# Optimization experiments

Hardware: AMD Instinct MI355X
Metric: run time of the kernel (lower is better)

Reference implementation:

```python
import jax, jax.numpy as jnp
import numpy as np

N_NODES = 50000
N_EDGES = 1600000
IN_CH, HID_CH, OUT_CH = 256, 128, 64


def setup_inputs() -> dict:
    key = jax.random.key(0)
    k1, k2, k3, k4 = jax.random.split(key, 4)
    x = jax.random.normal(k1, (N_NODES, IN_CH), dtype=jnp.float32)
    edge_index = jax.random.randint(k2, (2, N_EDGES), 0, N_NODES, dtype=jnp.int64)
    # Glorot-style init for weights, zero bias (as PyG GCNConv)
    W1 = jax.random.normal(k3, (IN_CH, HID_CH), dtype=jnp.float32) * (1.0 / np.sqrt(IN_CH))
    b1 = jnp.zeros((HID_CH,), dtype=jnp.float32)
    W2 = jax.random.normal(k4, (HID_CH, OUT_CH), dtype=jnp.float32) * (1.0 / np.sqrt(HID_CH))
    b2 = jnp.zeros((OUT_CH,), dtype=jnp.float32)
    return {"x": x, "edge_index": edge_index, "W1": W1, "b1": b1, "W2": W2, "b2": b2}


def _gcn_norm(edge_index, num_nodes):
    # PyG GCNConv default: add self-loops, symmetric normalization deg^-1/2 A deg^-1/2
    loop = jnp.arange(num_nodes, dtype=edge_index.dtype)
    src = jnp.concatenate([edge_index[0], loop])
    dst = jnp.concatenate([edge_index[1], loop])
    deg = jax.ops.segment_sum(jnp.ones_like(dst, dtype=jnp.float32), dst, num_segments=num_nodes)
    dinv = jnp.where(deg > 0, jax.lax.rsqrt(jnp.maximum(deg, 1.0)), 0.0)
    norm = dinv[src] * dinv[dst]  # [E + N]
    return src, dst, norm


def _gcn_conv(x, src, dst, norm, W, b, num_nodes):
    h = x @ W                              # [N, C_out] dense GEMM first (PyG order)
    msg = h[src] * norm[:, None]           # gather + scale, [E+N, C_out]
    out = jax.ops.segment_sum(msg, dst, num_segments=num_nodes)  # scatter-add
    return out + b


def reference(x, edge_index, W1, b1, W2, b2):
    n = x.shape[0]
    src, dst, norm = _gcn_norm(edge_index, n)
    h = _gcn_conv(x, src, dst, norm, W1, b1, n)
    h = jax.nn.relu(h)
    # F.dropout(training=self.training): eval mode -> identity
    h = _gcn_conv(h, src, dst, norm, W2, b2, n)
    return jax.nn.log_softmax(h, axis=1)
```

## Files before the change

### kernel.cpp

```cpp
#include <hip/hip_runtime.h>
#include <math.h>

#define NN 50000
#define NE 1600000
#define NBIN 391
#define BINW 128
#define STCAP 6144
#define OVFCAP 32768
#define NBLK 512
#define EPB 3125

typedef __attribute__((ext_vector_type(8))) short bf16x8;
typedef __attribute__((ext_vector_type(4))) float f32x4;
union frag_u { unsigned u[4]; bf16x8 v; };

__device__ __forceinline__ float blo(unsigned u) { return __uint_as_float(u << 16); }
__device__ __forceinline__ float bhi(unsigned u) { return __uint_as_float(u & 0xffff0000u); }
__device__ __forceinline__ unsigned bpack(float a, float b) {
    unsigned ua = __float_as_uint(a), ub = __float_as_uint(b);
    ua += 0x7fffu + ((ua >> 16) & 1u);
    ub += 0x7fffu + ((ub >> 16) & 1u);
    return (ua >> 16) | (ub & 0xffff0000u);
}
__device__ __forceinline__ unsigned short b16(float a) {
    unsigned ua = __float_as_uint(a);
    ua += 0x7fffu + ((ua >> 16) & 1u);
    return (unsigned short)(ua >> 16);
}

__device__ __forceinline__ int edge_get(const void* ei, int is64, long long i) {
    return is64 ? (int)((const long long*)ei)[i] : ((const int*)ei)[i];
}

__global__ void k_detect(const unsigned int* __restrict__ e, int* flag) {
    unsigned int v = e[2 * threadIdx.x + 1];
    unsigned long long m = __ballot(v != 0u);
    if (threadIdx.x == 0) *flag = (m == 0ull) ? 1 : 0;
}

__global__ __launch_bounds__(256) void k_bin(const void* __restrict__ ei,
                                             const int* __restrict__ flag,
                                             int* __restrict__ bincnt,
                                             unsigned* __restrict__ staged,
                                             int* __restrict__ ovfcnt,
                                             unsigned* __restrict__ ovf) {
    __shared__ unsigned lpk[EPB];
    __shared__ int lhist[NBIN], lbase[NBIN], lcur[NBIN];
    int is64 = *flag;
    int t = threadIdx.x;
    long long e0 = (long long)blockIdx.x * EPB;
    for (int i = t; i < NBIN; i += 256) { lhist[i] = 0; lcur[i] = 0; }
    __syncthreads();
    for (int j = t; j < EPB; j += 256) {
        int s = edge_get(ei, is64, e0 + j);
        int d = edge_get(ei, is64, (long long)NE + e0 + j);
        unsigned p = ((unsigned)d << 16) | (unsigned)s;
        lpk[j] = p;
        atomicAdd(&lhist[d >> 7], 1);
    }
    __syncthreads();
    for (int i = t; i < NBIN; i += 256)
        lbase[i] = (lhist[i] > 0) ? atomicAdd(&bincnt[i], lhist[i]) : 0;
    __syncthreads();
    for (int j = t; j < EPB; j += 256) {
        unsigned p = lpk[j];
        int bin = p >> 23;
        int pos = lbase[bin] + atomicAdd(&lcur[bin], 1);
        if (pos < STCAP) {
            staged[(long long)bin * STCAP + pos] = p;
        } else {
            int o = atomicAdd(ovfcnt, 1);
            if (o < OVFCAP) ovf[o] = p;
        }
    }
}

__global__ __launch_bounds__(512) void k_binscan(const int* __restrict__ bincnt,
                                                 int* __restrict__ binbase) {
    __shared__ int s[512];
    int t = threadIdx.x;
    int v = (t < NBIN) ? bincnt[t] : 0;
    s[t] = v;
    __syncthreads();
#pragma unroll
    for (int off = 1; off < 512; off <<= 1) {
        int u = (t >= off) ? s[t - off] : 0;
        __syncthreads();
        s[t] += u;
        __syncthreads();
    }
    if (t < NBIN) binbase[t] = s[t] - v;
}

__global__ __launch_bounds__(256) void k_csr(const unsigned* __restrict__ staged,
                                             const int* __restrict__ bincnt,
                                             const int* __restrict__ binbase,
                                             const int* __restrict__ ovfcnt,
                                             const unsigned* __restrict__ ovf,
                                             int* __restrict__ rowstart,
                                             int* __restrict__ cnt,
                                             float* __restrict__ dinv,
                                             int* __restrict__ csr) {
    __shared__ int lcnt[BINW], lpre[BINW], lcur[BINW];
    int b = blockIdx.x, t = threadIdx.x;
    int n = min(bincnt[b], STCAP);
    int novf = *ovfcnt;
    const unsigned* st = staged + (long long)b * STCAP;
    if (t < BINW) { lcnt[t] = 0; lcur[t] = 0; }
    __syncthreads();
    for (int j = t; j < n; j += 256) atomicAdd(&lcnt[(st[j] >> 16) & (BINW - 1)], 1);
    for (int j = t; j < novf; j += 256) {
        unsigned p = ovf[j];
        if ((int)(p >> 23) == b) atomicAdd(&lcnt[(p >> 16) & (BINW - 1)], 1);
    }
    __syncthreads();
    if (t < BINW) lpre[t] = lcnt[t];
    __syncthreads();
#pragma unroll
    for (int off = 1; off < BINW; off <<= 1) {
        int u = (t < BINW && t >= off) ? lpre[t - off] : 0;
        __syncthreads();
        if (t < BINW && t >= off) lpre[t] += u;
        __syncthreads();
    }
    int base = binbase[b];
    if (t < BINW) {
        int c = lcnt[t];
        int ex = lpre[t] - c;
        lpre[t] = ex;
        int node = b * BINW + t;
        if (node < NN) {
            rowstart[node] = base + ex;
            cnt[node] = c;
            dinv[node] = rsqrtf((float)c + 1.0f);
        }
    }
    __syncthreads();
    for (int j = t; j < n; j += 256) {
        unsigned p = st[j];
        int dloc = (p >> 16) & (BINW - 1);
        int pos = base + lpre[dloc] + atomicAdd(&lcur[dloc], 1);
        csr[pos] = (int)(p & 0xffffu);
    }
    for (int j = t; j < novf; j += 256) {
        unsigned p = ovf[j];
        if ((int)(p >> 23) == b) {
            int dloc = (p >> 16) & (BINW - 1);
            int pos = base + lpre[dloc] + atomicAdd(&lcur[dloc], 1);
            csr[pos] = (int)(p & 0xffffu);
        }
    }
}

__global__ __launch_bounds__(256) void k_mm1(const float* __restrict__ X,
                                             const float* __restrict__ W,
                                             const float* __restrict__ dinv,
                                             unsigned short* __restrict__ outh) {
    __shared__ unsigned short Wt[128][264];
    int tid = threadIdx.x;
    for (int idx = tid; idx < 128 * 256; idx += 256) {
        int col = idx & 127, k = idx >> 7;
        Wt[col][k] = b16(W[k * 128 + col]);
    }
    __syncthreads();
    int w = tid >> 6, l = tid & 63;
    int lr = l & 15, kg = l >> 4;
    int row = blockIdx.x * 64 + w * 16 + lr;
    long long rowc = min(row, NN - 1);
    f32x4 acc[8];
#pragma unroll
    for (int cf = 0; cf < 8; cf++) acc[cf] = {0.f, 0.f, 0.f, 0.f};
#pragma unroll
    for (int ks = 0; ks < 8; ks++) {
        int k0 = ks * 32 + kg * 8;
        const float4* p = (const float4*)(X + rowc * 256 + k0);
        float4 v0 = p[0], v1 = p[1];
        frag_u a;
        a.u[0] = bpack(v0.x, v0.y); a.u[1] = bpack(v0.z, v0.w);
        a.u[2] = bpack(v1.x, v1.y); a.u[3] = bpack(v1.z, v1.w);
#pragma unroll
        for (int cf = 0; cf < 8; cf++) {
            uint4 bb = *(const uint4*)&Wt[cf * 16 + lr][k0];
            frag_u b;
            b.u[0] = bb.x; b.u[1] = bb.y; b.u[2] = bb.z; b.u[3] = bb.w;
            acc[cf] = __builtin_amdgcn_mfma_f32_16x16x32_bf16(a.v, b.v, acc[cf], 0, 0, 0);
        }
    }
    int orow0 = blockIdx.x * 64 + w * 16 + kg * 4;
#pragma unroll
    for (int r = 0; r < 4; r++) {
        int orow = orow0 + r;
        if (orow < NN) {
            float s = dinv[orow];
#pragma unroll
            for (int cf = 0; cf < 8; cf++)
                outh[(long long)orow * 128 + cf * 16 + lr] = b16(s * acc[cf][r]);
        }
    }
}

__global__ __launch_bounds__(256) void k_mm2(const unsigned short* __restrict__ Xh,
                                             const float* __restrict__ W,
                                             const float* __restrict__ dinv,
                                             unsigned short* __restrict__ outh) {
    __shared__ unsigned short Wt[64][136];
    int tid = threadIdx.x;
    for (int idx = tid; idx < 64 * 128; idx += 256) {
        int col = idx & 63, k = idx >> 6;
        Wt[col][k] = b16(W[k * 64 + col]);
    }
    __syncthreads();
    int w = tid >> 6, l = tid & 63;
    int lr = l & 15, kg = l >> 4;
    int row = blockIdx.x * 64 + w * 16 + lr;
    long long rowc = min(row, NN - 1);
    f32x4 acc[4];
#pragma unroll
    for (int cf = 0; cf < 4; cf++) acc[cf] = {0.f, 0.f, 0.f, 0.f};
#pragma unroll
    for (int ks = 0; ks < 4; ks++) {
        int k0 = ks * 32 + kg * 8;
        uint4 av = *(const uint4*)(Xh + rowc * 128 + k0);
        frag_u a;
        a.u[0] = av.x; a.u[1] = av.y; a.u[2] = av.z; a.u[3] = av.w;
#pragma unroll
        for (int cf = 0; cf < 4; cf++) {
            uint4 bb = *(const uint4*)&Wt[cf * 16 + lr][k0];
            frag_u b;
            b.u[0] = bb.x; b.u[1] = bb.y; b.u[2] = bb.z; b.u[3] = bb.w;
            acc[cf] = __builtin_amdgcn_mfma_f32_16x16x32_bf16(a.v, b.v, acc[cf], 0, 0, 0);
        }
    }
    int orow0 = blockIdx.x * 64 + w * 16 + kg * 4;
#pragma unroll
    for (int r = 0; r < 4; r++) {
        int orow = orow0 + r;
        if (orow < NN) {
            float s = dinv[orow];
#pragma unroll
            for (int cf = 0; cf < 4; cf++)
                outh[(long long)orow * 64 + cf * 16 + lr] = b16(s * acc[cf][r]);
        }
    }
}

__global__ __launch_bounds__(256) void k_gather_relu(const uint4* __restrict__ h,
                                                     const int* __restrict__ csr,
                                                     const int* __restrict__ rowstart,
                                                     const int* __restrict__ cnt,
                                                     const float* __restrict__ dinv,
                                                     const float* __restrict__ bias,
                                                     uint4* __restrict__ out) {
    int tid = threadIdx.x;
    int node = blockIdx.x * 16 + (tid >> 4);
    int cl = tid & 15;
    if (node >= NN) return;
    int beg = rowstart[node], n = cnt[node];
    float acc[8];
    {
        uint4 v = h[(long long)node * 16 + cl];
        acc[0] = blo(v.x); acc[1] = bhi(v.x); acc[2] = blo(v.y); acc[3] = bhi(v.y);
        acc[4] = blo(v.z); acc[5] = bhi(v.z); acc[6] = blo(v.w); acc[7] = bhi(v.w);
    }
    int j = 0;
    for (; j + 3 < n; j += 4) {
        int a0 = csr[beg + j], a1 = csr[beg + j + 1];
        int a2 = csr[beg + j + 2], a3 = csr[beg + j + 3];
        uint4 v0 = h[(long long)a0 * 16 + cl], v1 = h[(long long)a1 * 16 + cl];
        uint4 v2 = h[(long long)a2 * 16 + cl], v3 = h[(long long)a3 * 16 + cl];
        acc[0] += blo(v0.x); acc[1] += bhi(v0.x); acc[2] += blo(v0.y); acc[3] += bhi(v0.y);
        acc[4] += blo(v0.z); acc[5] += bhi(v0.z); acc[6] += blo(v0.w); acc[7] += bhi(v0.w);
        acc[0] += blo(v1.x); acc[1] += bhi(v1.x); acc[2] += blo(v1.y); acc[3] += bhi(v1.y);
        acc[4] += blo(v1.z); acc[5] += bhi(v1.z); acc[6] += blo(v1.w); acc[7] += bhi(v1.w);
        acc[0] += blo(v2.x); acc[1] += bhi(v2.x); acc[2] += blo(v2.y); acc[3] += bhi(v2.y);
        acc[4] += blo(v2.z); acc[5] += bhi(v2.z); acc[6] += blo(v2.w); acc[7] += bhi(v2.w);
        acc[0] += blo(v3.x); acc[1] += bhi(v3.x); acc[2] += blo(v3.y); acc[3] += bhi(v3.y);
        acc[4] += blo(v3.z); acc[5] += bhi(v3.z); acc[6] += blo(v3.w); acc[7] += bhi(v3.w);
    }
    for (; j < n; j++) {
        uint4 v = h[(long long)csr[beg + j] * 16 + cl];
        acc[0] += blo(v.x); acc[1] += bhi(v.x); acc[2] += blo(v.y); acc[3] += bhi(v.y);
        acc[4] += blo(v.z); acc[5] += bhi(v.z); acc[6] += blo(v.w); acc[7] += bhi(v.w);
    }
    float d = dinv[node];
    float4 b0 = *(const float4*)&bias[cl * 8];
    float4 b1 = *(const float4*)&bias[cl * 8 + 4];
    float r0 = fmaxf(fmaf(d, acc[0], b0.x), 0.f), r1 = fmaxf(fmaf(d, acc[1], b0.y), 0.f);
    float r2 = fmaxf(fmaf(d, acc[2], b0.z), 0.f), r3 = fmaxf(fmaf(d, acc[3], b0.w), 0.f);
    float r4 = fmaxf(fmaf(d, acc[4], b1.x), 0.f), r5 = fmaxf(fmaf(d, acc[5], b1.y), 0.f);
    float r6 = fmaxf(fmaf(d, acc[6], b1.z), 0.f), r7 = fmaxf(fmaf(d, acc[7], b1.w), 0.f);
    uint4 o;
    o.x = bpack(r0, r1); o.y = bpack(r2, r3); o.z = bpack(r4, r5); o.w = bpack(r6, r7);
    out[(long long)node * 16 + cl] = o;
}

__global__ __launch_bounds__(256) void k_gather_lsm(const uint4* __restrict__ h,
                                                    const int* __restrict__ csr,
                                                    const int* __restrict__ rowstart,
                                                    const int* __restrict__ cnt,
                                                    const float* __restrict__ dinv,
                                                    const float* __restrict__ bias,
                                                    float* __restrict__ out) {
    int tid = threadIdx.x;
    int node = blockIdx.x * 32 + (tid >> 3);
    int cl = tid & 7;
    if (node >= NN) return;
    int beg = rowstart[node], n = cnt[node];
    float acc[8];
    {
        uint4 v = h[(long long)node * 8 + cl];
        acc[0] = blo(v.x); acc[1] = bhi(v.x); acc[2] = blo(v.y); acc[3] = bhi(v.y);
        acc[4] = blo(v.z); acc[5] = bhi(v.z); acc[6] = blo(v.w); acc[7] = bhi(v.w);
    }
    int j = 0;
    for (; j + 3 < n; j += 4) {
        int a0 = csr[beg + j], a1 = csr[beg + j + 1];
        int a2 = csr[beg + j + 2], a3 = csr[beg + j + 3];
        uint4 v0 = h[(long long)a0 * 8 + cl], v1 = h[(long long)a1 * 8 + cl];
        uint4 v2 = h[(long long)a2 * 8 + cl], v3 = h[(long long)a3 * 8 + cl];
        acc[0] += blo(v0.x); acc[1] += bhi(v0.x); acc[2] += blo(v0.y); acc[3] += bhi(v0.y);
        acc[4] += blo(v0.z); acc[5] += bhi(v0.z); acc[6] += blo(v0.w); acc[7] += bhi(v0.w);
        acc[0] += blo(v1.x); acc[1] += bhi(v1.x); acc[2] += blo(v1.y); acc[3] += bhi(v1.y);
        acc[4] += blo(v1.z); acc[5] += bhi(v1.z); acc[6] += blo(v1.w); acc[7] += bhi(v1.w);
        acc[0] += blo(v2.x); acc[1] += bhi(v2.x); acc[2] += blo(v2.y); acc[3] += bhi(v2.y);
        acc[4] += blo(v2.z); acc[5] += bhi(v2.z); acc[6] += blo(v2.w); acc[7] += bhi(v2.w);
        acc[0] += blo(v3.x); acc[1] += bhi(v3.x); acc[2] += blo(v3.y); acc[3] += bhi(v3.y);
        acc[4] += blo(v3.z); acc[5] += bhi(v3.z); acc[6] += blo(v3.w); acc[7] += bhi(v3.w);
    }
    for (; j < n; j++) {
        uint4 v = h[(long long)csr[beg + j] * 8 + cl];
        acc[0] += blo(v.x); acc[1] += bhi(v.x); acc[2] += blo(v.y); acc[3] += bhi(v.y);
        acc[4] += blo(v.z); acc[5] += bhi(v.z); acc[6] += blo(v.w); acc[7] += bhi(v.w);
    }
    float d = dinv[node];
    float4 b0 = *(const float4*)&bias[cl * 8];
    float4 b1 = *(const float4*)&bias[cl * 8 + 4];
    float t[8];
    t[0] = fmaf(d, acc[0], b0.x); t[1] = fmaf(d, acc[1], b0.y);
    t[2] = fmaf(d, acc[2], b0.z); t[3] = fmaf(d, acc[3], b0.w);
    t[4] = fmaf(d, acc[4], b1.x); t[5] = fmaf(d, acc[5], b1.y);
    t[6] = fmaf(d, acc[6], b1.z); t[7] = fmaf(d, acc[7], b1.w);
    float m = t[0];
#pragma unroll
    for (int i = 1; i < 8; i++) m = fmaxf(m, t[i]);
#pragma unroll
    for (int o = 1; o < 8; o <<= 1) m = fmaxf(m, __shfl_xor(m, o));
    float ex = 0.f;
#pragma unroll
    for (int i = 0; i < 8; i++) ex += __expf(t[i] - m);
#pragma unroll
    for (int o = 1; o < 8; o <<= 1) ex += __shfl_xor(ex, o);
    float l = logf(ex);
    float4 w0 = {t[0] - m - l, t[1] - m - l, t[2] - m - l, t[3] - m - l};
    float4 w1 = {t[4] - m - l, t[5] - m - l, t[6] - m - l, t[7] - m - l};
    *(float4*)&out[(long long)node * 64 + cl * 8] = w0;
    *(float4*)&out[(long long)node * 64 + cl * 8 + 4] = w1;
}

extern "C" void kernel_launch(void* const* d_in, const int* in_sizes, int n_in,
                              void* d_out, int out_size, void* d_ws, size_t ws_size,
                              hipStream_t stream) {
    const float* x  = (const float*)d_in[0];
    const void*  ei = d_in[1];
    const float* W1 = (const float*)d_in[2];
    const float* b1 = (const float*)d_in[3];
    const float* W2 = (const float*)d_in[4];
    const float* b2 = (const float*)d_in[5];
    float* out = (float*)d_out;

    char* ws = (char*)d_ws;
    float*          dinv     = (float*)   (ws + 0x000000);
    int*            flag     = (int*)     (ws + 0x040000);
    int*            cnt      = (int*)     (ws + 0x050000);
    int*            rowstart = (int*)     (ws + 0x090000);
    int*            bincnt   = (int*)     (ws + 0x0D0000);
    int*            ovfcnt   = (int*)     (ws + 0x0D0000 + NBIN * 4);
    int*            binbase  = (int*)     (ws + 0x0D2000);
    unsigned*       ovf      = (unsigned*)(ws + 0x0E0000);
    int*            csr      = (int*)     (ws + 0x120000);
    unsigned short* h1       = (unsigned short*)(ws + 0x740000);
    unsigned short* out1     = (unsigned short*)(ws + 0x1400000);
    unsigned*       staged   = (unsigned*)(ws + 0x1400000);

    k_detect<<<1, 64, 0, stream>>>((const unsigned int*)ei, flag);
    hipMemsetAsync(bincnt, 0, (size_t)(NBIN + 1) * 4, stream);
    k_bin<<<NBLK, 256, 0, stream>>>(ei, flag, bincnt, staged, ovfcnt, ovf);
    k_binscan<<<1, 512, 0, stream>>>(bincnt, binbase);
    k_csr<<<NBIN, 256, 0, stream>>>(staged, bincnt, binbase, ovfcnt, ovf,
                                    rowstart, cnt, dinv, csr);

    k_mm1<<<(NN + 63) / 64, 256, 0, stream>>>(x, W1, dinv, h1);
    k_gather_relu<<<(NN + 15) / 16, 256, 0, stream>>>((const uint4*)h1, csr, rowstart, cnt,
                                                      dinv, b1, (uint4*)out1);

    k_mm2<<<(NN + 63) / 64, 256, 0, stream>>>(out1, W2, dinv, h1);
    k_gather_lsm<<<(NN + 31) / 32, 256, 0, stream>>>((const uint4*)h1, csr, rowstart, cnt,
                                                     dinv, b2, out);
}
```

Measured before the change: 247.6 us.

## Precompute bf16 weights once, fold bin scan into CSR, unroll gathers by 8

Adds a small kernel that converts and transposes W1 and W2 to bf16 once, so each matmul block reads B fragments from global/L2 instead of rebuilding a transposed copy in LDS per block. It removes the separate single-block bin-scan kernel by having each k_csr block reduce the preceding bin counts itself. The gather kernels get an 8-way unrolled edge loop to keep more loads in flight. Trade-offs: B fragments now come from global memory with strided access rather than LDS, and each CSR block does a redundant partial sum over the bin counts.

Measured after the change: 262.7 us. 1.06x slower.

```diff
diff --git a/kernel.cpp b/kernel.cpp
--- a/kernel.cpp
+++ b/kernel.cpp
@@ -27,6 +27,10 @@
     ua += 0x7fffu + ((ua >> 16) & 1u);
     return (unsigned short)(ua >> 16);
 }
+__device__ __forceinline__ void addrow(float* acc, uint4 v) {
+    acc[0] += blo(v.x); acc[1] += bhi(v.x); acc[2] += blo(v.y); acc[3] += bhi(v.y);
+    acc[4] += blo(v.z); acc[5] += bhi(v.z); acc[6] += blo(v.w); acc[7] += bhi(v.w);
+}
 
 __device__ __forceinline__ int edge_get(const void* ei, int is64, long long i) {
     return is64 ? (int)((const long long*)ei)[i] : ((const int*)ei)[i];
@@ -36,6 +40,22 @@
     unsigned int v = e[2 * threadIdx.x + 1];
     unsigned long long m = __ballot(v != 0u);
     if (threadIdx.x == 0) *flag = (m == 0ull) ? 1 : 0;
+}
+
+__global__ __launch_bounds__(256) void k_wcvt(const float* __restrict__ W1,
+                                              const float* __restrict__ W2,
+                                              unsigned short* __restrict__ Wt1,
+                                              unsigned short* __restrict__ Wt2) {
+    int idx = blockIdx.x * 256 + threadIdx.x;
+    if (idx < 128 * 256) {
+        int c = idx >> 8, k = idx & 255;
+        Wt1[idx] = b16(W1[(long long)k * 128 + c]);
+    }
+    idx -= 128 * 256;
+    if (idx >= 0 && idx < 64 * 128) {
+        int c = idx >> 7, k = idx & 127;
+        Wt2[idx] = b16(W2[(long long)k * 64 + c]);
+    }
 }
 
 __global__ __launch_bounds__(256) void k_bin(const void* __restrict__ ei,
@@ -75,26 +95,8 @@
     }
 }
 
-__global__ __launch_bounds__(512) void k_binscan(const int* __restrict__ bincnt,
-                                                 int* __restrict__ binbase) {
-    __shared__ int s[512];
-    int t = threadIdx.x;
-    int v = (t < NBIN) ? bincnt[t] : 0;
-    s[t] = v;
-    __syncthreads();
-#pragma unroll
-    for (int off = 1; off < 512; off <<= 1) {
-        int u = (t >= off) ? s[t - off] : 0;
-        __syncthreads();
-        s[t] += u;
-        __syncthreads();
-    }
-    if (t < NBIN) binbase[t] = s[t] - v;
-}
-
 __global__ __launch_bounds__(256) void k_csr(const unsigned* __restrict__ staged,
                                              const int* __restrict__ bincnt,
-                                             const int* __restrict__ binbase,
                                              const int* __restrict__ ovfcnt,
                                              const unsigned* __restrict__ ovf,
                                              int* __restrict__ rowstart,
@@ -102,7 +104,18 @@
                                              float* __restrict__ dinv,
                                              int* __restrict__ csr) {
     __shared__ int lcnt[BINW], lpre[BINW], lcur[BINW];
+    __shared__ int red[256];
     int b = blockIdx.x, t = threadIdx.x;
+    int part = 0;
+    for (int i = t; i < b; i += 256) part += bincnt[i];
+    red[t] = part;
+    __syncthreads();
+#pragma unroll
+    for (int off = 128; off; off >>= 1) {
+        if (t < off) red[t] += red[t + off];
+        __syncthreads();
+    }
+    int base = red[0];
     int n = min(bincnt[b], STCAP);
     int novf = *ovfcnt;
     const unsigned* st = staged + (long long)b * STCAP;
@@ -123,7 +136,6 @@
         if (t < BINW && t >= off) lpre[t] += u;
         __syncthreads();
     }
-    int base = binbase[b];
     if (t < BINW) {
         int c = lcnt[t];
         int ex = lpre[t] - c;
@@ -153,16 +165,10 @@
 }
 
 __global__ __launch_bounds__(256) void k_mm1(const float* __restrict__ X,
-                                             const float* __restrict__ W,
+                                             const unsigned short* __restrict__ Wt,
                                              const float* __restrict__ dinv,
                                              unsigned short* __restrict__ outh) {
-    __shared__ unsigned short Wt[128][264];
     int tid = threadIdx.x;
-    for (int idx = tid; idx < 128 * 256; idx += 256) {
-        int col = idx & 127, k = idx >> 7;
-        Wt[col][k] = b16(W[k * 128 + col]);
-    }
-    __syncthreads();
     int w = tid >> 6, l = tid & 63;
     int lr = l & 15, kg = l >> 4;
     int row = blockIdx.x * 64 + w * 16 + lr;
@@ -180,7 +186,7 @@
         a.u[2] = bpack(v1.x, v1.y); a.u[3] = bpack(v1.z, v1.w);
 #pragma unroll
         for (int cf = 0; cf < 8; cf++) {
-            uint4 bb = *(const uint4*)&Wt[cf * 16 + lr][k0];
+            uint4 bb = *(const uint4*)&Wt[(cf * 16 + lr) * 256 + k0];
             frag_u b;
             b.u[0] = bb.x; b.u[1] = bb.y; b.u[2] = bb.z; b.u[3] = bb.w;
             acc[cf] = __builtin_amdgcn_mfma_f32_16x16x32_bf16(a.v, b.v, acc[cf], 0, 0, 0);
@@ -200,16 +206,10 @@
 }
 
 __global__ __launch_bounds__(256) void k_mm2(const unsigned short* __restrict__ Xh,
-                                             const float* __restrict__ W,
+                                             const unsigned short* __restrict__ Wt,
                                              const float* __restrict__ dinv,
                                              unsigned short* __restrict__ outh) {
-    __shared__ unsigned short Wt[64][136];
     int tid = threadIdx.x;
-    for (int idx = tid; idx < 64 * 128; idx += 256) {
-        int col = idx & 63, k = idx >> 6;
-        Wt[col][k] = b16(W[k * 64 + col]);
-    }
-    __syncthreads();
     int w = tid >> 6, l = tid & 63;
     int lr = l & 15, kg = l >> 4;
     int row = blockIdx.x * 64 + w * 16 + lr;
@@ -225,7 +225,7 @@
         a.u[0] = av.x; a.u[1] = av.y; a.u[2] = av.z; a.u[3] = av.w;
 #pragma unroll
         for (int cf = 0; cf < 4; cf++) {
-            uint4 bb = *(const uint4*)&Wt[cf * 16 + lr][k0];
+            uint4 bb = *(const uint4*)&Wt[(cf * 16 + lr) * 128 + k0];
             frag_u b;
             b.u[0] = bb.x; b.u[1] = bb.y; b.u[2] = bb.z; b.u[3] = bb.w;
             acc[cf] = __builtin_amdgcn_mfma_f32_16x16x32_bf16(a.v, b.v, acc[cf], 0, 0, 0);
@@ -263,25 +263,26 @@
         acc[4] = blo(v.z); acc[5] = bhi(v.z); acc[6] = blo(v.w); acc[7] = bhi(v.w);
     }
     int j = 0;
+    for (; j + 7 < n; j += 8) {
+        int a0 = csr[beg + j + 0], a1 = csr[beg + j + 1];
+        int a2 = csr[beg + j + 2], a3 = csr[beg + j + 3];
+        int a4 = csr[beg + j + 4], a5 = csr[beg + j + 5];
+        int a6 = csr[beg + j + 6], a7 = csr[beg + j + 7];
+        uint4 v0 = h[(long long)a0 * 16 + cl], v1 = h[(long long)a1 * 16 + cl];
+        uint4 v2 = h[(long long)a2 * 16 + cl], v3 = h[(long long)a3 * 16 + cl];
+        uint4 v4 = h[(long long)a4 * 16 + cl], v5 = h[(long long)a5 * 16 + cl];
+        uint4 v6 = h[(long long)a6 * 16 + cl], v7 = h[(long long)a7 * 16 + cl];
+        addrow(acc, v0); addrow(acc, v1); addrow(acc, v2); addrow(acc, v3);
+        addrow(acc, v4); addrow(acc, v5); addrow(acc, v6); addrow(acc, v7);
+    }
     for (; j + 3 < n; j += 4) {
-        int a0 = csr[beg + j], a1 = csr[beg + j + 1];
+        int a0 = csr[beg + j + 0], a1 = csr[beg + j + 1];
         int a2 = csr[beg + j + 2], a3 = csr[beg + j + 3];
         uint4 v0 = h[(long long)a0 * 16 + cl], v1 = h[(long long)a1 * 16 + cl];
         uint4 v2 = h[(long long)a2 * 16 + cl], v3 = h[(long long)a3 * 16 + cl];
-        acc[0] += blo(v0.x); acc[1] += bhi(v0.x); acc[2] += blo(v0.y); acc[3] += bhi(v0.y);
-        acc[4] += blo(v0.z); acc[5] += bhi(v0.z); acc[6] += blo(v0.w); acc[7] += bhi(v0.w);
-        acc[0] += blo(v1.x); acc[1] += bhi(v1.x); acc[2] += blo(v1.y); acc[3] += bhi(v1.y);
-        acc[4] += blo(v1.z); acc[5] += bhi(v1.z); acc[6] += blo(v1.w); acc[7] += bhi(v1.w);
-        acc[0] += blo(v2.x); acc[1] += bhi(v2.x); acc[2] += blo(v2.y); acc[3] += bhi(v2.y);
-        acc[4] += blo(v2.z); acc[5] += bhi(v2.z); acc[6] += blo(v2.w); acc[7] += bhi(v2.w);
-        acc[0] += blo(v3.x); acc[1] += bhi(v3.x); acc[2] += blo(v3.y); acc[3] += bhi(v3.y);
-        acc[4] += blo(v3.z); acc[5] += bhi(v3.z); acc[6] += blo(v3.w); acc[7] += bhi(v3.w);
-    }
-    for (; j < n; j++) {
-        uint4 v = h[(long long)csr[beg + j] * 16 + cl];
-        acc[0] += blo(v.x); acc[1] += bhi(v.x); acc[2] += blo(v.y); acc[3] += bhi(v.y);
-        acc[4] += blo(v.z); acc[5] += bhi(v.z); acc[6] += blo(v.w); acc[7] += bhi(v.w);
-    }
+        addrow(acc, v0); addrow(acc, v1); addrow(acc, v2); addrow(acc, v3);
+    }
+    for (; j < n; j++) addrow(acc, h[(long long)csr[beg + j] * 16 + cl]);
     float d = dinv[node];
     float4 b0 = *(const float4*)&bias[cl * 8];
     float4 b1 = *(const float4*)&bias[cl * 8 + 4];
@@ -313,25 +314,26 @@
         acc[4] = blo(v.z); acc[5] = bhi(v.z); acc[6] = blo(v.w); acc[7] = bhi(v.w);
     }
     int j = 0;
+    for (; j + 7 < n; j += 8) {
+        int a0 = csr[beg + j + 0], a1 = csr[beg + j + 1];
+        int a2 = csr[beg + j + 2], a3 = csr[beg + j + 3];
+        int a4 = csr[beg + j + 4], a5 = csr[beg + j + 5];
+        int a6 = csr[beg + j + 6], a7 = csr[beg + j + 7];
+        uint4 v0 = h[(long long)a0 * 8 + cl], v1 = h[(long long)a1 * 8 + cl];
+        uint4 v2 = h[(long long)a2 * 8 + cl], v3 = h[(long long)a3 * 8 + cl];
+        uint4 v4 = h[(long long)a4 * 8 + cl], v5 = h[(long long)a5 * 8 + cl];
+        uint4 v6 = h[(long long)a6 * 8 + cl], v7 = h[(long long)a7 * 8 + cl];
+        addrow(acc, v0); addrow(acc, v1); addrow(acc, v2); addrow(acc, v3);
+        addrow(acc, v4); addrow(acc, v5); addrow(acc, v6); addrow(acc, v7);
+    }
     for (; j + 3 < n; j += 4) {
-        int a0 = csr[beg + j], a1 = csr[beg + j + 1];
+        int a0 = csr[beg + j + 0], a1 = csr[beg + j + 1];
         int a2 = csr[beg + j + 2], a3 = csr[beg + j + 3];
         uint4 v0 = h[(long long)a0 * 8 + cl], v1 = h[(long long)a1 * 8 + cl];
         uint4 v2 = h[(long long)a2 * 8 + cl], v3 = h[(long long)a3 * 8 + cl];
-        acc[0] += blo(v0.x); acc[1] += bhi(v0.x); acc[2] += blo(v0.y); acc[3] += bhi(v0.y);
-        acc[4] += blo(v0.z); acc[5] += bhi(v0.z); acc[6] += blo(v0.w); acc[7] += bhi(v0.w);
-        acc[0] += blo(v1.x); acc[1] += bhi(v1.x); acc[2] += blo(v1.y); acc[3] += bhi(v1.y);
-        acc[4] += blo(v1.z); acc[5] += bhi(v1.z); acc[6] += blo(v1.w); acc[7] += bhi(v1.w);
-        acc[0] += blo(v2.x); acc[1] += bhi(v2.x); acc[2] += blo(v2.y); acc[3] += bhi(v2.y);
-        acc[4] += blo(v2.z); acc[5] += bhi(v2.z); acc[6] += blo(v2.w); acc[7] += bhi(v2.w);
-        acc[0] += blo(v3.x); acc[1] += bhi(v3.x); acc[2] += blo(v3.y); acc[3] += bhi(v3.y);
-        acc[4] += blo(v3.z); acc[5] += bhi(v3.z); acc[6] += blo(v3.w); acc[7] += bhi(v3.w);
-    }
-    for (; j < n; j++) {
-        uint4 v = h[(long long)csr[beg + j] * 8 + cl];
-        acc[0] += blo(v.x); acc[1] += bhi(v.x); acc[2] += blo(v.y); acc[3] += bhi(v.y);
-        acc[4] += blo(v.z); acc[5] += bhi(v.z); acc[6] += blo(v.w); acc[7] += bhi(v.w);
-    }
+        addrow(acc, v0); addrow(acc, v1); addrow(acc, v2); addrow(acc, v3);
+    }
+    for (; j < n; j++) addrow(acc, h[(long long)csr[beg + j] * 8 + cl]);
     float d = dinv[node];
     float4 b0 = *(const float4*)&bias[cl * 8];
     float4 b1 = *(const float4*)&bias[cl * 8 + 4];
@@ -375,25 +377,25 @@
     int*            rowstart = (int*)     (ws + 0x090000);
     int*            bincnt   = (int*)     (ws + 0x0D0000);
     int*            ovfcnt   = (int*)     (ws + 0x0D0000 + NBIN * 4);
-    int*            binbase  = (int*)     (ws + 0x0D2000);
     unsigned*       ovf      = (unsigned*)(ws + 0x0E0000);
     int*            csr      = (int*)     (ws + 0x120000);
-    unsigned short* h1       = (unsigned short*)(ws + 0x740000);
+    unsigned short* Wt1      = (unsigned short*)(ws + 0x740000);
+    unsigned short* Wt2      = (unsigned short*)(ws + 0x750000);
+    unsigned short* h1       = (unsigned short*)(ws + 0x760000);
     unsigned short* out1     = (unsigned short*)(ws + 0x1400000);
     unsigned*       staged   = (unsigned*)(ws + 0x1400000);
 
     k_detect<<<1, 64, 0, stream>>>((const unsigned int*)ei, flag);
+    k_wcvt<<<(128 * 256 + 64 * 128 + 255) / 256, 256, 0, stream>>>(W1, W2, Wt1, Wt2);
     hipMemsetAsync(bincnt, 0, (size_t)(NBIN + 1) * 4, stream);
     k_bin<<<NBLK, 256, 0, stream>>>(ei, flag, bincnt, staged, ovfcnt, ovf);
-    k_binscan<<<1, 512, 0, stream>>>(bincnt, binbase);
-    k_csr<<<NBIN, 256, 0, stream>>>(staged, bincnt, binbase, ovfcnt, ovf,
-                                    rowstart, cnt, dinv, csr);
-
-    k_mm1<<<(NN + 63) / 64, 256, 0, stream>>>(x, W1, dinv, h1);
+    k_csr<<<NBIN, 256, 0, stream>>>(staged, bincnt, ovfcnt, ovf, rowstart, cnt, dinv, csr);
+
+    k_mm1<<<(NN + 63) / 64, 256, 0, stream>>>(x, Wt1, dinv, h1);
     k_gather_relu<<<(NN + 15) / 16, 256, 0, stream>>>((const uint4*)h1, csr, rowstart, cnt,
                                                       dinv, b1, (uint4*)out1);
 
-    k_mm2<<<(NN + 63) / 64, 256, 0, stream>>>(out1, W2, dinv, h1);
+    k_mm2<<<(NN + 63) / 64, 256, 0, stream>>>(out1, Wt2, dinv, h1);
     k_gather_lsm<<<(NN + 31) / 32, 256, 0, stream>>>((const uint4*)h1, csr, rowstart, cnt,
                                                      dinv, b2, out);
 }
```
